# Kernel optimization log

Measured on AMD Instinct MI355X. Metric: run time of the kernel, lower is better.

The kernel has to match this reference:

```python
import jax, jax.numpy as jnp
import numpy as np

B, CIN, CH, COUT = 16, 256, 256, 256
RES = 16
E = 32           # embed_dim
NEMB = 1024      # codebook size
NP = 128         # n_phylo_channels (ch - NP == NP)
L = 4            # n_phylolevels
K = 8            # attribute codes per level per kernel
KN = 32          # nonattribute codes per kernel (levels=1)
CP = L * K * E   # 1024 projected phylo channels
CN = KN * E      # 1024 projected nonattr channels
BETA = 0.25
EPS = 1e-5

def conv1x1(x, w, b):
    # x: [B,C,H,W], w: [O,C], b: [O]
    return jnp.einsum('oc,bchw->bohw', w, x) + b[None, :, None, None]

def layernorm_chw(x, w, b):
    # LayerNorm over (C,H,W) per sample, elementwise affine of shape [C,H,W]
    mu = jnp.mean(x, axis=(1, 2, 3), keepdims=True)
    var = jnp.var(x, axis=(1, 2, 3), keepdims=True)
    return (x - mu) * jax.lax.rsqrt(var + EPS) * w[None] + b[None]

def reshape_in(x, levels):
    # [B, E*levels*K', H, W] -> [B, E, K'*H*W, levels]
    Bb, C, H, W = x.shape
    Kp = C // (E * levels)
    x = x.reshape(Bb, E, levels, Kp, H * W)
    x = x.transpose(0, 1, 3, 4, 2)          # [B,E,K',HW,levels]
    return x.reshape(Bb, E, Kp * H * W, levels)

def reshape_out(x, levels):
    # [B, E, K'*HW, levels] -> [B, E*levels*K', RES, RES]
    Bb, Ee, N, Ll = x.shape
    Kp = N // (RES * RES)
    x = x.reshape(Bb, Ee, Kp, RES * RES, Ll)
    x = x.transpose(0, 1, 4, 2, 3)          # [B,E,levels,K',HW]
    return x.reshape(Bb, Ee * Ll * Kp, RES, RES)

def quantize(z, codebook):
    # z: [B, E, N, levels]; codebook: [NEMB, E]
    zp = z.transpose(0, 2, 3, 1)            # [B,N,levels,E]
    flat = zp.reshape(-1, E)
    d = (jnp.sum(flat * flat, axis=1, keepdims=True)
         - 2.0 * flat @ codebook.T
         + jnp.sum(codebook * codebook, axis=1)[None, :])
    idx = jnp.argmin(d, axis=1)
    zq = codebook[idx].reshape(zp.shape)
    sg = jax.lax.stop_gradient
    loss = jnp.mean((sg(zq) - zp) ** 2) + BETA * jnp.mean((zq - sg(zp)) ** 2)
    zq = zp + sg(zq - zp)                   # straight-through
    return zq.transpose(0, 3, 1, 2), loss

def setup_inputs() -> dict:
    key = jax.random.key(0)
    ks = jax.random.split(key, 20)
    s = 0.02
    inp = {
        'x': jax.random.normal(ks[0], (B, CIN, RES, RES), jnp.float32),
        'conv_in_w': jax.random.normal(ks[1], (CH, CIN), jnp.float32) * s,
        'conv_in_b': jnp.zeros((CH,), jnp.float32),
        'ln_p_w': jnp.ones((NP, RES, RES), jnp.float32),
        'ln_p_b': jnp.zeros((NP, RES, RES), jnp.float32),
        'wp_in': jax.random.normal(ks[2], (CP, NP), jnp.float32) * s,
        'bp_in': jnp.zeros((CP,), jnp.float32),
        'wp_out': jax.random.normal(ks[3], (NP, CP), jnp.float32) * s,
        'bp_out': jnp.zeros((NP,), jnp.float32),
        'ln_n_w': jnp.ones((CH - NP, RES, RES), jnp.float32),
        'ln_n_b': jnp.zeros((CH - NP, RES, RES), jnp.float32),
        'wn_in': jax.random.normal(ks[4], (CN, CH - NP), jnp.float32) * s,
        'bn_in': jnp.zeros((CN,), jnp.float32),
        'wn_out': jax.random.normal(ks[5], (CH - NP, CN), jnp.float32) * s,
        'bn_out': jnp.zeros((CH - NP,), jnp.float32),
        'codebook': jax.random.uniform(ks[6], (NEMB, E), jnp.float32,
                                       -1.0 / NEMB, 1.0 / NEMB),
        'conv_out_w': jax.random.normal(ks[7], (COUT, CH), jnp.float32) * s,
        'conv_out_b': jnp.zeros((COUT,), jnp.float32),
    }
    return inp

def reference(x, conv_in_w, conv_in_b, ln_p_w, ln_p_b, wp_in, bp_in,
              wp_out, bp_out, ln_n_w, ln_n_b, wn_in, bn_in, wn_out, bn_out,
              codebook, conv_out_w, conv_out_b):
    silu = jax.nn.silu
    h = conv1x1(silu(x), conv_in_w, conv_in_b)
    h_p, h_n = h[:, :NP], h[:, NP:]
    # phylo branch
    z_p = silu(conv1x1(layernorm_chw(silu(h_p), ln_p_w, ln_p_b), wp_in, bp_in))
    zq_p, loss_p = quantize(reshape_in(z_p, L), codebook)
    hout_p = silu(conv1x1(reshape_out(zq_p, L), wp_out, bp_out))
    # non-attribute branch (anticlassification path)
    z_n = silu(conv1x1(layernorm_chw(silu(h_n), ln_n_w, ln_n_b), wn_in, bn_in))
    zq_n, loss_n = quantize(reshape_in(z_n, 1), codebook)
    hout_n = silu(conv1x1(reshape_out(zq_n, 1), wn_out, bn_out))
    h_cat = jnp.concatenate([hout_p, hout_n], axis=1)
    out = conv1x1(silu(h_cat), conv_out_w, conv_out_b)
    return out, loss_p + loss_n, zq_p
```

## Files before the change

### kernel.cpp

```cpp
#include <hip/hip_runtime.h>
#include <hip/hip_bf16.h>


typedef float f32x4  __attribute__((ext_vector_type(4)));
typedef short bf16x8 __attribute__((ext_vector_type(8)));

__device__ __forceinline__ float silu_rw(float x){ return x / (1.f + expf(-x)); }
__device__ __forceinline__ float b2f_rw(__hip_bfloat16 v){ return __bfloat162float(v); }
__device__ __forceinline__ float ldv_rw(const void* p, int i, int f32m){
  if (f32m) return ((const float*)p)[i];
  return b2f_rw(((const __hip_bfloat16*)p)[i]);
}
__device__ __forceinline__ unsigned short f2bf_rw(float x){
  unsigned u = __float_as_uint(x);
  unsigned r = ((u >> 16) & 1u) + 0x7FFFu;
  return (unsigned short)((u + r) >> 16);
}
__device__ __forceinline__ float bf2f_rw(unsigned short h){
  return __uint_as_float(((unsigned)h) << 16);
}

#define FLAGS_OFF 0
#define LOSS_OFF  4
#define STATS_OFF 8
#define CNT_OFF   72
#define CMAX_OFF  80
#define CB32_OFF  128
#define CBN_OFF   32896
#define IDXP_OFF  33984
#define IDXN_OFF  165056
#define CBHL_OFF  296192
#define LIST_OFF  328960
#define R2_OFF    460032
#define R3_OFF    984320
#define R1_OFF    1508608

__global__ __launch_bounds__(256) void detect_rw(const void* cbv, float* wsb){
  __shared__ int bad;
  if (threadIdx.x == 0) bad = 0;
  __syncthreads();
  const unsigned short* u = (const unsigned short*)cbv;
  int local = 0;
  for (int i = threadIdx.x; i < 32768; i += 256){
    unsigned e = (u[i] >> 7) & 0xFF;
    if (e >= 126) local = 1;
  }
  if (local) bad = 1;
  __syncthreads();
  if (threadIdx.x == 0){
    wsb[FLAGS_OFF] = bad ? 1.f : 0.f;
    wsb[LOSS_OFF] = 0.f; wsb[LOSS_OFF + 1] = 0.f;
    int* c = (int*)(wsb + CNT_OFF);
    #pragma unroll
    for (int k = 0; k < 8; ++k) c[k] = 0;
    wsb[CMAX_OFF] = 0.f;
  }
}

__global__ __launch_bounds__(256) void cbprep_rw(const void* cbv, const float* flags,
                                                 float* cb32, float* cbn,
                                                 short* cbhl, float* cmaxp){
  const int f32m = (flags[0] != 0.f);
  int j = blockIdx.x * 256 + threadIdx.x;
  if (j < 1024){
    float s = 0.f;
    const int tb = ((j >> 4) << 10) + ((j & 15) << 5);
    for (int e = 0; e < 32; ++e){
      float v = ldv_rw(cbv, j*32 + e, f32m);
      cb32[j*32 + e] = v;
      unsigned short h = f2bf_rw(v);
      cbhl[tb + e]       = (short)h;
      cbhl[tb + e + 512] = (short)f2bf_rw(v - bf2f_rw(h));
      s += v*v;
    }
    cbn[j] = s;
    atomicMax((int*)cmaxp, __float_as_int(sqrtf(s)));
  }
}

template<int KCH, int INMODE, bool OUTSILU, bool ATOMIC, int LEVELS>
__global__ __launch_bounds__(256) void gemm2_rw(
    const float* __restrict__ inF, const float* __restrict__ inF2,
    const void* __restrict__ inV,
    const void* __restrict__ W, const void* __restrict__ biasO,
    const void* __restrict__ sbA, const void* __restrict__ sbB,
    const int* __restrict__ idxin, const float* __restrict__ cb32,
    float* __restrict__ outF, const float* __restrict__ flags,
    int KDIM, int OUTC, int o_off, int b_base, int ib_sub, int ob_sub)
{
  __shared__ float As[32][32];
  __shared__ float Bs[32][68];

  const int f32m = (flags[0] != 0.f);
  const int t  = threadIdx.x;
  const int q0 = (blockIdx.x << 5) + (b_base << 8);
  const int b  = q0 >> 8;
  const int p0 = q0 & 255;
  const int o0 = blockIdx.y << 6;
  const int k0base = blockIdx.z * KCH;
  const int tx = t & 15, ty = t >> 4;
  float acc[4][2] = {};

  const int sch = t >> 3, spx = (t & 7) << 2;

  for (int kc = 0; kc < KCH; kc += 32){
    const int k0 = k0base + kc;
    if constexpr (INMODE == 0){
      const float4 v = *reinterpret_cast<const float4*>(
          &inF[(((b - ib_sub)*KDIM + k0 + sch) << 8) + p0 + spx]);
      *reinterpret_cast<float4*>(&As[sch][spx]) = v;
    } else if constexpr (INMODE == 2){
      if (f32m){
        const float* xf = (const float*)inV;
        float4 v = *reinterpret_cast<const float4*>(&xf[((b*KDIM + k0 + sch) << 8) + p0 + spx]);
        v.x = silu_rw(v.x); v.y = silu_rw(v.y); v.z = silu_rw(v.z); v.w = silu_rw(v.w);
        *reinterpret_cast<float4*>(&As[sch][spx]) = v;
      } else {
        const __hip_bfloat16* xb = (const __hip_bfloat16*)inV;
        const int off = ((b*KDIM + k0 + sch) << 8) + p0 + spx;
        #pragma unroll
        for (int j = 0; j < 4; ++j) As[sch][spx + j] = silu_rw(b2f_rw(xb[off + j]));
      }
    } else {
      const float* src = (k0 < 128) ? inF : inF2;
      const void* sb   = (k0 < 128) ? sbA : sbB;
      const int kh = k0 & 127;
      const float bb = ldv_rw(sb, kh + sch, f32m);
      float4 v = *reinterpret_cast<const float4*>(&src[((b*128 + kh + sch) << 8) + p0 + spx]);
      v.x = silu_rw(v.x + bb); v.y = silu_rw(v.y + bb);
      v.z = silu_rw(v.z + bb); v.w = silu_rw(v.w + bb);
      *reinterpret_cast<float4*>(&As[sch][spx]) = v;
    }
    if (f32m){
      const float* Wf = (const float*)W;
      #pragma unroll
      for (int r = 0; r < 8; ++r){
        int ii = t + (r << 8); int oo = ii >> 5, cc = ii & 31;
        Bs[cc][oo] = Wf[(o0 + oo)*KDIM + k0 + cc];
      }
    } else {
      const __hip_bfloat16* Wb = (const __hip_bfloat16*)W;
      #pragma unroll
      for (int r = 0; r < 8; ++r){
        int ii = t + (r << 8); int oo = ii >> 5, cc = ii & 31;
        Bs[cc][oo] = b2f_rw(Wb[(o0 + oo)*KDIM + k0 + cc]);
      }
    }
    __syncthreads();
    #pragma unroll
    for (int kk = 0; kk < 32; ++kk){
      const float2 a = *reinterpret_cast<const float2*>(&As[kk][tx << 1]);
      const float4 w = *reinterpret_cast<const float4*>(&Bs[kk][ty << 2]);
      acc[0][0] += w.x*a.x; acc[0][1] += w.x*a.y;
      acc[1][0] += w.y*a.x; acc[1][1] += w.y*a.y;
      acc[2][0] += w.z*a.x; acc[2][1] += w.z*a.y;
      acc[3][0] += w.w*a.x; acc[3][1] += w.w*a.y;
    }
    __syncthreads();
  }
  #pragma unroll
  for (int i = 0; i < 4; ++i){
    const int o = o0 + (ty << 2) + i;
    const int base = (((b - ob_sub)*OUTC + o_off + o) << 8) + p0 + (tx << 1);
    if constexpr (ATOMIC){
      atomicAdd(&outF[base + 0], acc[i][0]);
      atomicAdd(&outF[base + 1], acc[i][1]);
    } else {
      const float bb = ldv_rw(biasO, o, f32m);
      float v0 = acc[i][0] + bb, v1 = acc[i][1] + bb;
      if constexpr (OUTSILU){ v0 = silu_rw(v0); v1 = silu_rw(v1); }
      *reinterpret_cast<float2*>(&outF[base]) = make_float2(v0, v1);
    }
  }
}

__global__ __launch_bounds__(256) void wprep_rw(const void* Wp, const void* Wn,
    const float* flags, short* whlp, short* whln){
  const int f32m = (flags[0] != 0.f);
  const void* W = blockIdx.y ? Wn : Wp;
  short* whl = blockIdx.y ? whln : whlp;
  const int t = threadIdx.x;
  const int sch = t & 31, o = (blockIdx.x << 3) + (t >> 5);
  const int ob = ((sch << 7) + o) << 6;
  for (int e = 0; e < 32; ++e){
    const float wv = ldv_rw(W, (o << 10) + (e << 5) + sch, f32m);
    const unsigned short h = f2bf_rw(wv);
    whl[ob + e]      = (short)h;
    whl[ob + 32 + e] = (short)f2bf_rw(wv - bf2f_rw(h));
  }
}

template<int LEVELS>
__global__ __launch_bounds__(256, 4) void houtm2_rw(
    const int* __restrict__ idxin, const short* __restrict__ cbhl,
    const short* __restrict__ whl, float* __restrict__ outF)
{
  const int t = threadIdx.x;
  const int lane = t & 63, wid = t >> 6;
  const int lc = lane & 15, gq = lane >> 4;
  const int b  = blockIdx.x >> 3;
  const int p0 = (blockIdx.x & 7) << 5;
  const int o0 = (blockIdx.y << 6) + (wid << 4);
  const int s0 = blockIdx.z << 3;
  const int ge = gq << 3;

  int j0[8], j1[8];
  #pragma unroll
  for (int s = 0; s < 8; ++s){
    const int sch = s0 + s;
    int a0, a1;
    if (LEVELS == 4){
      const int l = sch >> 3, kp = sch & 7;
      a0 = b*8192 + (((kp << 8) + p0 + lc) << 2) + l;
      a1 = b*8192 + (((kp << 8) + p0 + 16 + lc) << 2) + l;
    } else {
      a0 = b*8192 + (sch << 8) + p0 + lc;
      a1 = a0 + 16;
    }
    j0[s] = idxin[a0] & 1023;
    j1[s] = idxin[a1] & 1023;
  }

  f32x4 acc0 = {0.f, 0.f, 0.f, 0.f};
  f32x4 acc1 = {0.f, 0.f, 0.f, 0.f};

  #pragma unroll 1
  for (int s = 0; s < 8; ++s){
    const int sch = s0 + s;
    const int ja = j0[s], jb = j1[s];
    const int a0h = ((ja >> 4) << 10) + ((ja & 15) << 5) + ge;
    const int a1h = ((jb >> 4) << 10) + ((jb & 15) << 5) + ge;
    const bf16x8 ah0 = *reinterpret_cast<const bf16x8*>(cbhl + a0h);
    const bf16x8 al0 = *reinterpret_cast<const bf16x8*>(cbhl + a0h + 512);
    const bf16x8 ah1 = *reinterpret_cast<const bf16x8*>(cbhl + a1h);
    const bf16x8 al1 = *reinterpret_cast<const bf16x8*>(cbhl + a1h + 512);
    const int wb = (((sch << 7) + o0 + lc) << 6) + ge;
    const bf16x8 bh = *reinterpret_cast<const bf16x8*>(whl + wb);
    const bf16x8 bl = *reinterpret_cast<const bf16x8*>(whl + wb + 32);

    acc0 = __builtin_amdgcn_mfma_f32_16x16x32_bf16(ah0, bh, acc0, 0, 0, 0);
    acc0 = __builtin_amdgcn_mfma_f32_16x16x32_bf16(ah0, bl, acc0, 0, 0, 0);
    acc0 = __builtin_amdgcn_mfma_f32_16x16x32_bf16(al0, bh, acc0, 0, 0, 0);
    acc1 = __builtin_amdgcn_mfma_f32_16x16x32_bf16(ah1, bh, acc1, 0, 0, 0);
    acc1 = __builtin_amdgcn_mfma_f32_16x16x32_bf16(ah1, bl, acc1, 0, 0, 0);
    acc1 = __builtin_amdgcn_mfma_f32_16x16x32_bf16(al1, bh, acc1, 0, 0, 0);
  }

  const int obase = ((b*128 + o0 + lc) << 8) + p0 + (gq << 2);
  #pragma unroll
  for (int r = 0; r < 4; ++r){
    atomicAdd(&outF[obase + r],      acc0[r]);
    atomicAdd(&outF[obase + 16 + r], acc1[r]);
  }
}

__global__ __launch_bounds__(256) void stats_rw(const float* __restrict__ h, float* __restrict__ stats){
  const int b = blockIdx.x >> 1, half = blockIdx.x & 1;
  const float* base = h + ((b*256 + half*128) << 8);
  float s = 0.f, s2 = 0.f;
  for (int i = threadIdx.x; i < 32768; i += 256){
    float a = silu_rw(base[i]);
    s += a; s2 += a*a;
  }
  __shared__ float sh[2][256];
  sh[0][threadIdx.x] = s; sh[1][threadIdx.x] = s2;
  __syncthreads();
  for (int st = 128; st > 0; st >>= 1){
    if (threadIdx.x < st){
      sh[0][threadIdx.x] += sh[0][threadIdx.x + st];
      sh[1][threadIdx.x] += sh[1][threadIdx.x + st];
    }
    __syncthreads();
  }
  if (threadIdx.x == 0){
    float mu  = sh[0][0] * (1.f/32768.f);
    float var = sh[1][0] * (1.f/32768.f) - mu*mu;
    stats[half*32 + b]      = mu;
    stats[half*32 + 16 + b] = 1.f / sqrtf(var + 1e-5f);
  }
}

__global__ __launch_bounds__(256) void ln_rw(const float* __restrict__ h,
    const void* lwp, const void* lbp, const void* lwn, const void* lbn,
    const float* __restrict__ stats, const float* __restrict__ flags,
    float* __restrict__ lnp, float* __restrict__ lnn){
  const int f32m = (flags[0] != 0.f);
  int i = blockIdx.x * 256 + threadIdx.x;
  int b = i >> 16, c = (i >> 8) & 255, p = i & 255;
  float a = silu_rw(h[i]);
  if (c < 128){
    float v = (a - stats[b]) * stats[16 + b] * ldv_rw(lwp, (c << 8) + p, f32m) + ldv_rw(lbp, (c << 8) + p, f32m);
    lnp[((b*128 + c) << 8) + p] = v;
  } else {
    int cc = c - 128;
    float v = (a - stats[32 + b]) * stats[48 + b] * ldv_rw(lwn, (cc << 8) + p, f32m) + ldv_rw(lbn, (cc << 8) + p, f32m);
    lnn[((b*128 + cc) << 8) + p] = v;
  }
}

template<int LEVELS>
__global__ __launch_bounds__(512, 4) void quantm_rw(
    const float* __restrict__ z, const short* __restrict__ cbhl,
    const float* __restrict__ cbn, const float* __restrict__ cmaxp,
    int* __restrict__ idxout, float* __restrict__ lossacc,
    int* __restrict__ cnt, int* __restrict__ list, int b_base)
{
  __shared__ float mgm1[4][4][8], mgm2[4][4][8];
  __shared__ int   mgj [4][4][8];
  __shared__ float red[4];

  const int tid  = threadIdx.x;
  const int lane = tid & 63, wid = tid >> 6;
  const int lc = lane & 15, gq = lane >> 4;
  const int pg = wid & 3, ch = wid >> 2;
  const int bid  = blockIdx.x;
  const int bl   = bid >> 6;
  const int rest = bid & 63;
  const int g = rest >> 1, half = rest & 1;
  int cb, wbase, wstep;
  if (LEVELS == 4){ cb = (g & 3)*8 + (g >> 2); wbase = (g >> 2)*1024 + (g & 3); wstep = 4; }
  else            { cb = g;                    wbase = g << 8;                  wstep = 1; }
  const int pb = half*128 + pg*32;

  bf16x8 ah0, al0, ah1, al1;
  float zn0 = 0.f, zn1 = 0.f;
  const int zoff = (((bl << 10) + cb) << 8) + pb + lc;
  const int e0 = gq << 3;
  #pragma unroll
  for (int i = 0; i < 8; ++i){
    const int zo = zoff + ((e0 + i) << 13);
    const float z0 = z[zo];
    const float z1 = z[zo + 16];
    zn0 += z0*z0; zn1 += z1*z1;
    const float s0 = -2.f*z0, s1 = -2.f*z1;
    const unsigned short h0 = f2bf_rw(s0);
    const unsigned short h1 = f2bf_rw(s1);
    ah0[i] = (short)h0; al0[i] = (short)f2bf_rw(s0 - bf2f_rw(h0));
    ah1[i] = (short)h1; al1[i] = (short)f2bf_rw(s1 - bf2f_rw(h1));
  }
  zn0 += __shfl_xor(zn0, 16); zn0 += __shfl_xor(zn0, 32);
  zn1 += __shfl_xor(zn1, 16); zn1 += __shfl_xor(zn1, 32);

  float m1[8], m2[8]; int j1[8];
  #pragma unroll
  for (int s = 0; s < 8; ++s){ m1[s] = __builtin_inff(); m2[s] = __builtin_inff(); j1[s] = 0; }

  const short* bp  = cbhl + (ch << 15) + (lc << 5) + (gq << 3);
  const float* cnp = cbn + (ch << 9) + lc;

  bf16x8 bh  = *reinterpret_cast<const bf16x8*>(bp);
  bf16x8 blo = *reinterpret_cast<const bf16x8*>(bp + 512);
  float  cnv = cnp[0];

  #pragma unroll 2
  for (int t = 0; t < 32; ++t){
    const int tn = (t < 31) ? t + 1 : 31;
    const bf16x8 bhn  = *reinterpret_cast<const bf16x8*>(bp + (tn << 10));
    const bf16x8 blon = *reinterpret_cast<const bf16x8*>(bp + (tn << 10) + 512);
    const float  cnn  = cnp[tn << 4];

    f32x4 a0 = {cnv, cnv, cnv, cnv};
    f32x4 a1 = {cnv, cnv, cnv, cnv};
    a0 = __builtin_amdgcn_mfma_f32_16x16x32_bf16(ah0, bh,  a0, 0, 0, 0);
    a0 = __builtin_amdgcn_mfma_f32_16x16x32_bf16(ah0, blo, a0, 0, 0, 0);
    a0 = __builtin_amdgcn_mfma_f32_16x16x32_bf16(al0, bh,  a0, 0, 0, 0);
    a1 = __builtin_amdgcn_mfma_f32_16x16x32_bf16(ah1, bh,  a1, 0, 0, 0);
    a1 = __builtin_amdgcn_mfma_f32_16x16x32_bf16(ah1, blo, a1, 0, 0, 0);
    a1 = __builtin_amdgcn_mfma_f32_16x16x32_bf16(al1, bh,  a1, 0, 0, 0);

    const int jc = (((ch << 5) + t) << 4) + lc;
    #pragma unroll
    for (int r = 0; r < 4; ++r){
      const float d0 = a0[r];
      m2[r] = __builtin_amdgcn_fmed3f(d0, m1[r], m2[r]);
      const bool t0 = d0 < m1[r];
      j1[r] = t0 ? jc : j1[r]; m1[r] = t0 ? d0 : m1[r];
      const float d1 = a1[r];
      m2[4+r] = __builtin_amdgcn_fmed3f(d1, m1[4+r], m2[4+r]);
      const bool t1 = d1 < m1[4+r];
      j1[4+r] = t1 ? jc : j1[4+r]; m1[4+r] = t1 ? d1 : m1[4+r];
    }
    bh = bhn; blo = blon; cnv = cnn;
  }

  #pragma unroll
  for (int k = 1; k < 16; k <<= 1){
    #pragma unroll
    for (int s = 0; s < 8; ++s){
      const float om1 = __shfl_xor(m1[s], k);
      const float om2 = __shfl_xor(m2[s], k);
      const int   oj  = __shfl_xor(j1[s], k);
      m2[s] = fminf(fminf(m2[s], om2), fmaxf(m1[s], om1));
      const bool tk = (om1 < m1[s]) || (om1 == m1[s] && oj < j1[s]);
      m1[s] = tk ? om1 : m1[s];
      j1[s] = tk ? oj  : j1[s];
    }
  }

  if (wid >= 4 && lc == 0){
    #pragma unroll
    for (int s = 0; s < 8; ++s){
      mgm1[wid-4][gq][s] = m1[s];
      mgm2[wid-4][gq][s] = m2[s];
      mgj [wid-4][gq][s] = j1[s];
    }
  }
  __syncthreads();
  if (wid < 4){
    #pragma unroll
    for (int s = 0; s < 8; ++s){
      const float om1 = mgm1[wid][gq][s];
      const float om2 = mgm2[wid][gq][s];
      const int   oj  = mgj [wid][gq][s];
      m2[s] = fminf(fminf(m2[s], om2), fmaxf(m1[s], om1));
      const bool tk = om1 < m1[s];
      m1[s] = tk ? om1 : m1[s];
      j1[s] = tk ? oj  : j1[s];
    }

    const float cmax = cmaxp[0];
    float lossw = 0.f;
    #pragma unroll
    for (int f = 0; f < 2; ++f){
      #pragma unroll
      for (int r = 0; r < 4; ++r){
        const int s = f*4 + r;
        const int vrow = (gq << 2) + r;
        const float znv = __shfl(f == 0 ? zn0 : zn1, vrow);
        if (lc == 0){
          const int p  = pb + f*16 + vrow;
          const int gi = (b_base + bl)*8192 + wbase + p*wstep;
          idxout[gi] = j1[s];
          const float eb = fmaf(2.0e-6f, znv, 3.0e-4f * sqrtf(znv) * cmax);
          if (m2[s] - m1[s] > eb){
            lossw += znv + m1[s];
          } else {
            const int pos = atomicAdd(cnt, 1);
            if (pos < 131072) list[pos] = (((bl << 5) | g) << 8) | p;
          }
        }
      }
    }
    lossw += __shfl_xor(lossw, 16);
    lossw += __shfl_xor(lossw, 32);
    if (lane == 0) red[wid] = lossw;
  }
  __syncthreads();
  if (tid == 0) atomicAdd(lossacc, red[0] + red[1] + red[2] + red[3]);
}

template<int LEVELS>
__global__ __launch_bounds__(256) void fb_rw(
    const float* __restrict__ z, const float* __restrict__ cb32,
    const float* __restrict__ cbn, const int* __restrict__ cnt,
    const int* __restrict__ list, int* __restrict__ idxout,
    float* __restrict__ lossacc, int b_base)
{
  const int lane = threadIdx.x & 63;
  const int wv = (blockIdx.x << 2) | (threadIdx.x >> 6);
  const int nw = gridDim.x << 2;
  int n = cnt[0];
  if (n > 131072) n = 131072;
  for (int it = wv; it < n; it += nw){
    const int id = list[it];
    const int p = id & 255, g = (id >> 8) & 31, bl = id >> 13;
    int cb, w;
    if (LEVELS == 4){ cb = (g & 3)*8 + (g >> 2); w = (g >> 2)*1024 + (p << 2) + (g & 3); }
    else            { cb = g;                    w = (g << 8) + p; }
    const int zoff = (((bl << 10) + cb) << 8) + p;
    float myz = 0.f;
    if (lane < 32) myz = z[zoff + (lane << 13)];
    float zb[32];
    #pragma unroll
    for (int e = 0; e < 32; ++e) zb[e] = __shfl(myz, e);
    float zn = 0.f;
    #pragma unroll
    for (int e = 0; e < 32; ++e) zn = fmaf(zb[e], zb[e], zn);
    float bd = __builtin_inff(); int bj = 0;
    #pragma unroll 4
    for (int jj = 0; jj < 16; ++jj){
      const int j = (jj << 6) + lane;
      const float4* c4 = reinterpret_cast<const float4*>(cb32 + (j << 5));
      float dot = 0.f;
      #pragma unroll
      for (int e4 = 0; e4 < 8; ++e4){
        const float4 cv = c4[e4];
        dot = fmaf(zb[(e4 << 2) + 0], cv.x, dot);
        dot = fmaf(zb[(e4 << 2) + 1], cv.y, dot);
        dot = fmaf(zb[(e4 << 2) + 2], cv.z, dot);
        dot = fmaf(zb[(e4 << 2) + 3], cv.w, dot);
      }
      const float d = (zn - 2.f*dot) + cbn[j];
      if (d < bd){ bd = d; bj = j; }
    }
    #pragma unroll
    for (int k = 1; k < 64; k <<= 1){
      const float od = __shfl_xor(bd, k);
      const int   oj = __shfl_xor(bj, k);
      if (od < bd || (od == bd && oj < bj)){ bd = od; bj = oj; }
    }
    if (lane == 0){
      idxout[(b_base + bl)*8192 + w] = bj;
      atomicAdd(lossacc, bd);
    }
  }
}

__global__ __launch_bounds__(256) void zqout_rw(const int* __restrict__ idxp,
    const float* __restrict__ cb32, float* __restrict__ out){
  int t = blockIdx.x * 256 + threadIdx.x;
  int l = t & 3, n = (t >> 2) & 2047, e = (t >> 13) & 31, b = t >> 18;
  int id = idxp[b*8192 + (n << 2) + l];
  out[t] = cb32[((id & 1023) << 5) + e];
}

__global__ __launch_bounds__(256) void zero_rw(float* __restrict__ p){
  p[blockIdx.x * 256 + threadIdx.x] = 0.f;
}

__global__ void loss_rw(const float* __restrict__ lossacc, float* __restrict__ out){
  if (threadIdx.x == 0 && blockIdx.x == 0)
    out[0] = 1.25f * (lossacc[0] + lossacc[1]) * (1.f/4194304.f);
}

extern "C" void kernel_launch(void* const* d_in, const int* in_sizes, int n_in,
                              void* d_out, int out_size, void* d_ws, size_t ws_size,
                              hipStream_t stream){
  (void)in_sizes; (void)n_in; (void)out_size;
  const void* x   = d_in[0];
  const void* ciw = d_in[1];
  const void* cib = d_in[2];
  const void* lwp = d_in[3];
  const void* lbp = d_in[4];
  const void* wpi = d_in[5];
  const void* bpi = d_in[6];
  const void* wpo = d_in[7];
  const void* bpo = d_in[8];
  const void* lwn = d_in[9];
  const void* lbn = d_in[10];
  const void* wni = d_in[11];
  const void* bni = d_in[12];
  const void* wno = d_in[13];
  const void* bno = d_in[14];
  const void* cbk = d_in[15];
  const void* cow = d_in[16];
  const void* cob = d_in[17];

  float* ws    = (float*)d_ws;
  float* flags = ws + FLAGS_OFF;
  float* loss  = ws + LOSS_OFF;
  float* stats = ws + STATS_OFF;
  float* cmaxp = ws + CMAX_OFF;
  float* cb32  = ws + CB32_OFF;
  float* cbn   = ws + CBN_OFF;
  int*   cnts  = (int*)(ws + CNT_OFF);
  int*   idxp  = (int*)(ws + IDXP_OFF);
  int*   idxn  = (int*)(ws + IDXN_OFF);
  short* cbhl  = (short*)(ws + CBHL_OFF);
  int*   list  = (int*)(ws + LIST_OFF);
  float* R2    = ws + R2_OFF;
  float* R3    = ws + R3_OFF;
  float* R1    = ws + R1_OFF;
  short* whlp  = (short*)(ws + R1_OFF);
  short* whln  = (short*)(ws + R1_OFF + 131072);

  float* outO = (float*)d_out;
  float* outL = outO + 1048576;
  float* outZ = outO + 1048577;

  const size_t wsf = ws_size / 4;
  int CS = 4;
  if      (wsf >= (size_t)R1_OFF + 16u*262144u) CS = 16;
  else if (wsf >= (size_t)R1_OFF +  8u*262144u) CS = 8;

  detect_rw<<<1, 256, 0, stream>>>(cbk, ws);
  cbprep_rw<<<4, 256, 0, stream>>>(cbk, flags, cb32, cbn, cbhl, cmaxp);
  gemm2_rw<256,2,false,false,0><<<dim3(128,4), 256, 0, stream>>>(
      nullptr, nullptr, x, ciw, cib, nullptr, nullptr, nullptr, nullptr,
      R1, flags, 256, 256, 0, 0, 0, 0);
  stats_rw<<<32, 256, 0, stream>>>(R1, stats);
  ln_rw<<<4096, 256, 0, stream>>>(R1, lwp, lbp, lwn, lbn, stats, flags, R2, R3);
  {
    int ci = 0;
    for (int c = 0; c < 16; c += CS, ++ci){
      gemm2_rw<128,0,true,false,0><<<dim3(CS*8,16), 256, 0, stream>>>(
          R2, nullptr, nullptr, wpi, bpi, nullptr, nullptr, nullptr, nullptr,
          R1, flags, 128, 1024, 0, c, 0, c);
      quantm_rw<4><<<CS*64, 512, 0, stream>>>(R1, cbhl, cbn, cmaxp,
                                              idxp, loss + 0, cnts + ci, list, c);
      fb_rw<4><<<640, 256, 0, stream>>>(R1, cb32, cbn, cnts + ci, list,
                                        idxp, loss + 0, c);
    }
  }
  {
    int ci = 4;
    for (int c = 0; c < 16; c += CS, ++ci){
      gemm2_rw<128,0,true,false,0><<<dim3(CS*8,16), 256, 0, stream>>>(
          R3, nullptr, nullptr, wni, bni, nullptr, nullptr, nullptr, nullptr,
          R1, flags, 128, 1024, 0, c, 0, c);
      quantm_rw<1><<<CS*64, 512, 0, stream>>>(R1, cbhl, cbn, cmaxp,
                                              idxn, loss + 1, cnts + ci, list, c);
      fb_rw<1><<<640, 256, 0, stream>>>(R1, cb32, cbn, cnts + ci, list,
                                        idxn, loss + 1, c);
    }
  }
  zqout_rw<<<16384, 256, 0, stream>>>(idxp, cb32, outZ);
  zero_rw<<<4096, 256, 0, stream>>>(R2);
  wprep_rw<<<dim3(16, 2), 256, 0, stream>>>(wpo, wno, flags, whlp, whln);
  houtm2_rw<4><<<dim3(128, 2, 4), 256, 0, stream>>>(idxp, cbhl, whlp, R2);
  houtm2_rw<1><<<dim3(128, 2, 4), 256, 0, stream>>>(idxn, cbhl, whln, R3);
  gemm2_rw<256,5,false,false,0><<<dim3(128,4), 256, 0, stream>>>(
      R2, R3, nullptr, cow, cob, bpo, bno, nullptr, nullptr,
      outO, flags, 256, 256, 0, 0, 0, 0);
  loss_rw<<<1, 64, 0, stream>>>(loss, outL);
}
```

Before: 568.4 us.

## Prefetch operands in MFMA loops, widen weight prep grid, clean up gemm template

In the output-projection MFMA kernel, the codebook and weight fragments for the next step are now loaded ahead of the current step's MFMAs. The quantize distance loop is restructured into a two-stage software pipeline so loads run two iterations ahead. The weight-prep kernel now launches one block per output row with coalesced reads instead of 16 blocks with strided loops. Unused template parameters and arguments are dropped from the fp32 GEMM, and its accumulation is written as explicit fma. Deeper prefetching raises register pressure, which may cut occupancy in the quantize kernel.

```diff
diff --git a/kernel.cpp b/kernel.cpp
--- a/kernel.cpp
+++ b/kernel.cpp
@@ -78,13 +78,12 @@
   }
 }
 
-template<int KCH, int INMODE, bool OUTSILU, bool ATOMIC, int LEVELS>
+template<int KCH, int INMODE, bool OUTSILU>
 __global__ __launch_bounds__(256) void gemm2_rw(
     const float* __restrict__ inF, const float* __restrict__ inF2,
     const void* __restrict__ inV,
     const void* __restrict__ W, const void* __restrict__ biasO,
     const void* __restrict__ sbA, const void* __restrict__ sbB,
-    const int* __restrict__ idxin, const float* __restrict__ cb32,
     float* __restrict__ outF, const float* __restrict__ flags,
     int KDIM, int OUTC, int o_off, int b_base, int ib_sub, int ob_sub)
 {
@@ -151,10 +150,10 @@
     for (int kk = 0; kk < 32; ++kk){
       const float2 a = *reinterpret_cast<const float2*>(&As[kk][tx << 1]);
       const float4 w = *reinterpret_cast<const float4*>(&Bs[kk][ty << 2]);
-      acc[0][0] += w.x*a.x; acc[0][1] += w.x*a.y;
-      acc[1][0] += w.y*a.x; acc[1][1] += w.y*a.y;
-      acc[2][0] += w.z*a.x; acc[2][1] += w.z*a.y;
-      acc[3][0] += w.w*a.x; acc[3][1] += w.w*a.y;
+      acc[0][0] = fmaf(w.x, a.x, acc[0][0]); acc[0][1] = fmaf(w.x, a.y, acc[0][1]);
+      acc[1][0] = fmaf(w.y, a.x, acc[1][0]); acc[1][1] = fmaf(w.y, a.y, acc[1][1]);
+      acc[2][0] = fmaf(w.z, a.x, acc[2][0]); acc[2][1] = fmaf(w.z, a.y, acc[2][1]);
+      acc[3][0] = fmaf(w.w, a.x, acc[3][0]); acc[3][1] = fmaf(w.w, a.y, acc[3][1]);
     }
     __syncthreads();
   }
@@ -162,15 +161,10 @@
   for (int i = 0; i < 4; ++i){
     const int o = o0 + (ty << 2) + i;
     const int base = (((b - ob_sub)*OUTC + o_off + o) << 8) + p0 + (tx << 1);
-    if constexpr (ATOMIC){
-      atomicAdd(&outF[base + 0], acc[i][0]);
-      atomicAdd(&outF[base + 1], acc[i][1]);
-    } else {
-      const float bb = ldv_rw(biasO, o, f32m);
-      float v0 = acc[i][0] + bb, v1 = acc[i][1] + bb;
-      if constexpr (OUTSILU){ v0 = silu_rw(v0); v1 = silu_rw(v1); }
-      *reinterpret_cast<float2*>(&outF[base]) = make_float2(v0, v1);
-    }
+    const float bb = ldv_rw(biasO, o, f32m);
+    float v0 = acc[i][0] + bb, v1 = acc[i][1] + bb;
+    if constexpr (OUTSILU){ v0 = silu_rw(v0); v1 = silu_rw(v1); }
+    *reinterpret_cast<float2*>(&outF[base]) = make_float2(v0, v1);
   }
 }
 
@@ -179,14 +173,16 @@
   const int f32m = (flags[0] != 0.f);
   const void* W = blockIdx.y ? Wn : Wp;
   short* whl = blockIdx.y ? whln : whlp;
-  const int t = threadIdx.x;
-  const int sch = t & 31, o = (blockIdx.x << 3) + (t >> 5);
-  const int ob = ((sch << 7) + o) << 6;
-  for (int e = 0; e < 32; ++e){
-    const float wv = ldv_rw(W, (o << 10) + (e << 5) + sch, f32m);
+  const int o = blockIdx.x, t = threadIdx.x;
+  #pragma unroll
+  for (int ch = 0; ch < 4; ++ch){
+    const int k = (ch << 8) + t;
+    const int e = k >> 5, sch = k & 31;
+    const float wv = ldv_rw(W, (o << 10) + k, f32m);
     const unsigned short h = f2bf_rw(wv);
-    whl[ob + e]      = (short)h;
-    whl[ob + 32 + e] = (short)f2bf_rw(wv - bf2f_rw(h));
+    const int ob = (((sch << 7) + o) << 6) + e;
+    whl[ob]      = (short)h;
+    whl[ob + 32] = (short)f2bf_rw(wv - bf2f_rw(h));
   }
 }
 
@@ -224,19 +220,28 @@
   f32x4 acc0 = {0.f, 0.f, 0.f, 0.f};
   f32x4 acc1 = {0.f, 0.f, 0.f, 0.f};
 
+  int a0h = ((j0[0] >> 4) << 10) + ((j0[0] & 15) << 5) + ge;
+  int a1h = ((j1[0] >> 4) << 10) + ((j1[0] & 15) << 5) + ge;
+  int wb  = (((s0 << 7) + o0 + lc) << 6) + ge;
+  bf16x8 ah0 = *reinterpret_cast<const bf16x8*>(cbhl + a0h);
+  bf16x8 al0 = *reinterpret_cast<const bf16x8*>(cbhl + a0h + 512);
+  bf16x8 ah1 = *reinterpret_cast<const bf16x8*>(cbhl + a1h);
+  bf16x8 al1 = *reinterpret_cast<const bf16x8*>(cbhl + a1h + 512);
+  bf16x8 bh  = *reinterpret_cast<const bf16x8*>(whl + wb);
+  bf16x8 bl  = *reinterpret_cast<const bf16x8*>(whl + wb + 32);
+
   #pragma unroll 1
   for (int s = 0; s < 8; ++s){
-    const int sch = s0 + s;
-    const int ja = j0[s], jb = j1[s];
-    const int a0h = ((ja >> 4) << 10) + ((ja & 15) << 5) + ge;
-    const int a1h = ((jb >> 4) << 10) + ((jb & 15) << 5) + ge;
-    const bf16x8 ah0 = *reinterpret_cast<const bf16x8*>(cbhl + a0h);
-    const bf16x8 al0 = *reinterpret_cast<const bf16x8*>(cbhl + a0h + 512);
-    const bf16x8 ah1 = *reinterpret_cast<const bf16x8*>(cbhl + a1h);
-    const bf16x8 al1 = *reinterpret_cast<const bf16x8*>(cbhl + a1h + 512);
-    const int wb = (((sch << 7) + o0 + lc) << 6) + ge;
-    const bf16x8 bh = *reinterpret_cast<const bf16x8*>(whl + wb);
-    const bf16x8 bl = *reinterpret_cast<const bf16x8*>(whl + wb + 32);
+    const int sn = (s < 7) ? s + 1 : 7;
+    const int n0h = ((j0[sn] >> 4) << 10) + ((j0[sn] & 15) << 5) + ge;
+    const int n1h = ((j1[sn] >> 4) << 10) + ((j1[sn] & 15) << 5) + ge;
+    const int nwb = ((((s0 + sn) << 7) + o0 + lc) << 6) + ge;
+    const bf16x8 nah0 = *reinterpret_cast<const bf16x8*>(cbhl + n0h);
+    const bf16x8 nal0 = *reinterpret_cast<const bf16x8*>(cbhl + n0h + 512);
+    const bf16x8 nah1 = *reinterpret_cast<const bf16x8*>(cbhl + n1h);
+    const bf16x8 nal1 = *reinterpret_cast<const bf16x8*>(cbhl + n1h + 512);
+    const bf16x8 nbh  = *reinterpret_cast<const bf16x8*>(whl + nwb);
+    const bf16x8 nbl  = *reinterpret_cast<const bf16x8*>(whl + nwb + 32);
 
     acc0 = __builtin_amdgcn_mfma_f32_16x16x32_bf16(ah0, bh, acc0, 0, 0, 0);
     acc0 = __builtin_amdgcn_mfma_f32_16x16x32_bf16(ah0, bl, acc0, 0, 0, 0);
@@ -244,6 +249,8 @@
     acc1 = __builtin_amdgcn_mfma_f32_16x16x32_bf16(ah1, bh, acc1, 0, 0, 0);
     acc1 = __builtin_amdgcn_mfma_f32_16x16x32_bf16(ah1, bl, acc1, 0, 0, 0);
     acc1 = __builtin_amdgcn_mfma_f32_16x16x32_bf16(al1, bh, acc1, 0, 0, 0);
+
+    ah0 = nah0; al0 = nal0; ah1 = nah1; al1 = nal1; bh = nbh; bl = nbl;
   }
 
   const int obase = ((b*128 + o0 + lc) << 8) + p0 + (gq << 2);
@@ -348,39 +355,73 @@
   const short* bp  = cbhl + (ch << 15) + (lc << 5) + (gq << 3);
   const float* cnp = cbn + (ch << 9) + lc;
 
-  bf16x8 bh  = *reinterpret_cast<const bf16x8*>(bp);
-  bf16x8 blo = *reinterpret_cast<const bf16x8*>(bp + 512);
-  float  cnv = cnp[0];
-
-  #pragma unroll 2
-  for (int t = 0; t < 32; ++t){
-    const int tn = (t < 31) ? t + 1 : 31;
-    const bf16x8 bhn  = *reinterpret_cast<const bf16x8*>(bp + (tn << 10));
-    const bf16x8 blon = *reinterpret_cast<const bf16x8*>(bp + (tn << 10) + 512);
-    const float  cnn  = cnp[tn << 4];
-
-    f32x4 a0 = {cnv, cnv, cnv, cnv};
-    f32x4 a1 = {cnv, cnv, cnv, cnv};
-    a0 = __builtin_amdgcn_mfma_f32_16x16x32_bf16(ah0, bh,  a0, 0, 0, 0);
-    a0 = __builtin_amdgcn_mfma_f32_16x16x32_bf16(ah0, blo, a0, 0, 0, 0);
-    a0 = __builtin_amdgcn_mfma_f32_16x16x32_bf16(al0, bh,  a0, 0, 0, 0);
-    a1 = __builtin_amdgcn_mfma_f32_16x16x32_bf16(ah1, bh,  a1, 0, 0, 0);
-    a1 = __builtin_amdgcn_mfma_f32_16x16x32_bf16(ah1, blo, a1, 0, 0, 0);
-    a1 = __builtin_amdgcn_mfma_f32_16x16x32_bf16(al1, bh,  a1, 0, 0, 0);
-
-    const int jc = (((ch << 5) + t) << 4) + lc;
-    #pragma unroll
-    for (int r = 0; r < 4; ++r){
-      const float d0 = a0[r];
-      m2[r] = __builtin_amdgcn_fmed3f(d0, m1[r], m2[r]);
-      const bool t0 = d0 < m1[r];
-      j1[r] = t0 ? jc : j1[r]; m1[r] = t0 ? d0 : m1[r];
-      const float d1 = a1[r];
-      m2[4+r] = __builtin_amdgcn_fmed3f(d1, m1[4+r], m2[4+r]);
-      const bool t1 = d1 < m1[4+r];
-      j1[4+r] = t1 ? jc : j1[4+r]; m1[4+r] = t1 ? d1 : m1[4+r];
-    }
-    bh = bhn; blo = blon; cnv = cnn;
+  bf16x8 p0h = *reinterpret_cast<const bf16x8*>(bp);
+  bf16x8 p0l = *reinterpret_cast<const bf16x8*>(bp + 512);
+  float  p0c = cnp[0];
+  bf16x8 p1h = *reinterpret_cast<const bf16x8*>(bp + 1024);
+  bf16x8 p1l = *reinterpret_cast<const bf16x8*>(bp + 1024 + 512);
+  float  p1c = cnp[16];
+
+  #pragma unroll 1
+  for (int t = 0; t < 32; t += 2){
+    {
+      const int tn = (t + 2 < 32) ? t + 2 : 31;
+      const bf16x8 nh = *reinterpret_cast<const bf16x8*>(bp + (tn << 10));
+      const bf16x8 nl = *reinterpret_cast<const bf16x8*>(bp + (tn << 10) + 512);
+      const float  nc = cnp[tn << 4];
+
+      f32x4 a0 = {p0c, p0c, p0c, p0c};
+      f32x4 a1 = {p0c, p0c, p0c, p0c};
+      a0 = __builtin_amdgcn_mfma_f32_16x16x32_bf16(ah0, p0h, a0, 0, 0, 0);
+      a0 = __builtin_amdgcn_mfma_f32_16x16x32_bf16(ah0, p0l, a0, 0, 0, 0);
+      a0 = __builtin_amdgcn_mfma_f32_16x16x32_bf16(al0, p0h, a0, 0, 0, 0);
+      a1 = __builtin_amdgcn_mfma_f32_16x16x32_bf16(ah1, p0h, a1, 0, 0, 0);
+      a1 = __builtin_amdgcn_mfma_f32_16x16x32_bf16(ah1, p0l, a1, 0, 0, 0);
+      a1 = __builtin_amdgcn_mfma_f32_16x16x32_bf16(al1, p0h, a1, 0, 0, 0);
+
+      const int jc = (((ch << 5) + t) << 4) + lc;
+      #pragma unroll
+      for (int r = 0; r < 4; ++r){
+        const float d0 = a0[r];
+        m2[r] = __builtin_amdgcn_fmed3f(d0, m1[r], m2[r]);
+        const bool t0 = d0 < m1[r];
+        j1[r] = t0 ? jc : j1[r]; m1[r] = t0 ? d0 : m1[r];
+        const float d1 = a1[r];
+        m2[4+r] = __builtin_amdgcn_fmed3f(d1, m1[4+r], m2[4+r]);
+        const bool t1 = d1 < m1[4+r];
+        j1[4+r] = t1 ? jc : j1[4+r]; m1[4+r] = t1 ? d1 : m1[4+r];
+      }
+      p0h = nh; p0l = nl; p0c = nc;
+    }
+    {
+      const int tn = (t + 3 < 32) ? t + 3 : 31;
+      const bf16x8 nh = *reinterpret_cast<const bf16x8*>(bp + (tn << 10));
+      const bf16x8 nl = *reinterpret_cast<const bf16x8*>(bp + (tn << 10) + 512);
+      const float  nc = cnp[tn << 4];
+
+      f32x4 a0 = {p1c, p1c, p1c, p1c};
+      f32x4 a1 = {p1c, p1c, p1c, p1c};
+      a0 = __builtin_amdgcn_mfma_f32_16x16x32_bf16(ah0, p1h, a0, 0, 0, 0);
+      a0 = __builtin_amdgcn_mfma_f32_16x16x32_bf16(ah0, p1l, a0, 0, 0, 0);
+      a0 = __builtin_amdgcn_mfma_f32_16x16x32_bf16(al0, p1h, a0, 0, 0, 0);
+      a1 = __builtin_amdgcn_mfma_f32_16x16x32_bf16(ah1, p1h, a1, 0, 0, 0);
+      a1 = __builtin_amdgcn_mfma_f32_16x16x32_bf16(ah1, p1l, a1, 0, 0, 0);
+      a1 = __builtin_amdgcn_mfma_f32_16x16x32_bf16(al1, p1h, a1, 0, 0, 0);
+
+      const int jc = (((ch << 5) + t + 1) << 4) + lc;
+      #pragma unroll
+      for (int r = 0; r < 4; ++r){
+        const float d0 = a0[r];
+        m2[r] = __builtin_amdgcn_fmed3f(d0, m1[r], m2[r]);
+        const bool t0 = d0 < m1[r];
+        j1[r] = t0 ? jc : j1[r]; m1[r] = t0 ? d0 : m1[r];
+        const float d1 = a1[r];
+        m2[4+r] = __builtin_amdgcn_fmed3f(d1, m1[4+r], m2[4+r]);
+        const bool t1 = d1 < m1[4+r];
+        j1[4+r] = t1 ? jc : j1[4+r]; m1[4+r] = t1 ? d1 : m1[4+r];
+      }
+      p1h = nh; p1l = nl; p1c = nc;
+    }
   }
 
   #pragma unroll
@@ -575,16 +616,16 @@
 
   detect_rw<<<1, 256, 0, stream>>>(cbk, ws);
   cbprep_rw<<<4, 256, 0, stream>>>(cbk, flags, cb32, cbn, cbhl, cmaxp);
-  gemm2_rw<256,2,false,false,0><<<dim3(128,4), 256, 0, stream>>>(
-      nullptr, nullptr, x, ciw, cib, nullptr, nullptr, nullptr, nullptr,
+  gemm2_rw<256,2,false><<<dim3(128,4), 256, 0, stream>>>(
+      nullptr, nullptr, x, ciw, cib, nullptr, nullptr,
       R1, flags, 256, 256, 0, 0, 0, 0);
   stats_rw<<<32, 256, 0, stream>>>(R1, stats);
   ln_rw<<<4096, 256, 0, stream>>>(R1, lwp, lbp, lwn, lbn, stats, flags, R2, R3);
   {
     int ci = 0;
     for (int c = 0; c < 16; c += CS, ++ci){
-      gemm2_rw<128,0,true,false,0><<<dim3(CS*8,16), 256, 0, stream>>>(
-          R2, nullptr, nullptr, wpi, bpi, nullptr, nullptr, nullptr, nullptr,
+      gemm2_rw<128,0,true><<<dim3(CS*8,16), 256, 0, stream>>>(
+          R2, nullptr, nullptr, wpi, bpi, nullptr, nullptr,
           R1, flags, 128, 1024, 0, c, 0, c);
       quantm_rw<4><<<CS*64, 512, 0, stream>>>(R1, cbhl, cbn, cmaxp,
                                               idxp, loss + 0, cnts + ci, list, c);
@@ -595,8 +636,8 @@
   {
     int ci = 4;
     for (int c = 0; c < 16; c += CS, ++ci){
-      gemm2_rw<128,0,true,false,0><<<dim3(CS*8,16), 256, 0, stream>>>(
-          R3, nullptr, nullptr, wni, bni, nullptr, nullptr, nullptr, nullptr,
+      gemm2_rw<128,0,true><<<dim3(CS*8,16), 256, 0, stream>>>(
+          R3, nullptr, nullptr, wni, bni, nullptr, nullptr,
           R1, flags, 128, 1024, 0, c, 0, c);
       quantm_rw<1><<<CS*64, 512, 0, stream>>>(R1, cbhl, cbn, cmaxp,
                                               idxn, loss + 1, cnts + ci, list, c);
@@ -606,11 +647,11 @@
   }
   zqout_rw<<<16384, 256, 0, stream>>>(idxp, cb32, outZ);
   zero_rw<<<4096, 256, 0, stream>>>(R2);
-  wprep_rw<<<dim3(16, 2), 256, 0, stream>>>(wpo, wno, flags, whlp, whln);
+  wprep_rw<<<dim3(128, 2), 256, 0, stream>>>(wpo, wno, flags, whlp, whln);
   houtm2_rw<4><<<dim3(128, 2, 4), 256, 0, stream>>>(idxp, cbhl, whlp, R2);
   houtm2_rw<1><<<dim3(128, 2, 4), 256, 0, stream>>>(idxn, cbhl, whln, R3);
-  gemm2_rw<256,5,false,false,0><<<dim3(128,4), 256, 0, stream>>>(
-      R2, R3, nullptr, cow, cob, bpo, bno, nullptr, nullptr,
+  gemm2_rw<256,5,false><<<dim3(128,4), 256, 0, stream>>>(
+      R2, R3, nullptr, cow, cob, bpo, bno,
       outO, flags, 256, 256, 0, 0, 0, 0);
   loss_rw<<<1, 64, 0, stream>>>(loss, outL);
 }
```

Result: no change. 561.3 us (-1.3%).
